# Kernel optimization log

Hardware: AMD Instinct MI355X
Metric: run time of the kernel (lower is better)

Reference implementation:

```python
import jax, jax.numpy as jnp
import numpy as np
import math

B, HW, E = 128, 3136, 96
NH, WS = 3, 7
EH = E // NH
NEG_INF = float('-inf')


def setup_inputs() -> dict:
    key = jax.random.key(0)
    ks = jax.random.split(key, 5)
    x = jax.random.normal(ks[0], (B, HW, E), dtype=jnp.float32)
    w1 = jax.random.normal(ks[1], (3 * E, E), dtype=jnp.float32) * 0.02
    b1 = jnp.zeros((3 * E,), dtype=jnp.float32)
    w2 = jax.random.normal(ks[2], (E, E), dtype=jnp.float32) * 0.02
    b2 = jnp.zeros((E,), dtype=jnp.float32)
    return {"x": x, "w1": w1, "b1": b1, "w2": w2, "b2": b2}


def _masks():
    m = WS * (WS // 2)  # 21
    row = jnp.zeros((WS * WS, WS * WS), dtype=jnp.float32)
    row = row.at[-m:, :-m].set(NEG_INF)
    row = row.at[:-m, -m:].set(NEG_INF)
    # rearrange '(r w1) (c w2) -> (w1 r) (w2 c)'
    col = row.reshape(WS, WS, WS, WS).transpose(1, 0, 3, 2).reshape(WS * WS, WS * WS)
    return row, col


def reference(x, w1, b1, w2, b2):
    b = x.shape[0]
    hh = ww = int(round(math.sqrt(x.shape[1])))
    nh, nw = hh // WS, ww // WS
    qkv = x @ w1.T + b1                      # [b, hw, 3E]
    qkv = qkv.reshape(b, hh, ww, E, 3)       # (c K) split, K=3
    # cyclic shift: (-WS)//2 == -4 (faithful to torch source)
    s = (-WS) // 2
    qkv = jnp.roll(qkv, (s, s), axis=(1, 2))
    # window partition: b (h m1) (w m2) (H E) K -> b H h w (m1 m2) E K
    t = qkv.reshape(b, nh, WS, nw, WS, NH, EH, 3)
    t = t.transpose(0, 5, 1, 3, 2, 4, 6, 7).reshape(b, NH, nh, nw, WS * WS, EH, 3)
    q, k, v = t[..., 0], t[..., 1], t[..., 2]
    att = jnp.einsum('bHxyqe,bHxyke->bHxyqk', q, k) / math.sqrt(EH)
    row_mask, col_mask = _masks()
    att = att.at[:, :, -1, :].add(row_mask)
    att = att.at[:, :, :, -1].add(col_mask)
    p = jax.nn.softmax(att, axis=-1)
    o = jnp.einsum('bHxyqk,bHxyke->bHxyqe', p, v)
    # reverse window partition: b H h w (m1 m2) E -> b (h m1) (w m2) (H E)
    o = o.reshape(b, NH, nh, nw, WS, WS, EH)
    o = o.transpose(0, 2, 4, 3, 5, 1, 6).reshape(b, hh, ww, E)
    o = jnp.roll(o, (WS // 2, WS // 2), axis=(1, 2))  # +3 (faithful)
    o = o.reshape(b, hh * ww, E)
    return o @ w2.T + b2
```

## Files before the change

kernel.cpp:

```cpp
#include <hip/hip_runtime.h>

typedef __attribute__((ext_vector_type(8))) __bf16 bf16x8;
typedef __attribute__((ext_vector_type(4))) float f32x4;
typedef __attribute__((ext_vector_type(4))) unsigned int u32x4;

__device__ __forceinline__ unsigned short f2bf(float f){
    unsigned int x = __builtin_bit_cast(unsigned int, f);
    x += 0x7FFFu + ((x >> 16) & 1u);
    return (unsigned short)(x >> 16);
}
__device__ __forceinline__ unsigned int pk2(float a, float b){
    return (unsigned int)f2bf(a) | ((unsigned int)f2bf(b) << 16);
}
__device__ __forceinline__ unsigned int cvtpk(float a, float b){
    unsigned int r;
    asm("v_cvt_pk_bf16_f32 %0, %1, %2" : "=v"(r) : "v"(a), "v"(b));
    return r;
}
__device__ __forceinline__ unsigned short cvt1(float a){
    return (unsigned short)(cvtpk(a, a) & 0xFFFFu);
}
__device__ __forceinline__ bf16x8 ldfrag(const unsigned short* p){
    u32x4 v = *reinterpret_cast<const u32x4*>(p);
    return __builtin_bit_cast(bf16x8, v);
}
__device__ __forceinline__ bf16x8 ldf32(const float* p){
    f32x4 a = *reinterpret_cast<const f32x4*>(p);
    f32x4 b = *reinterpret_cast<const f32x4*>(p + 4);
    u32x4 r;
    r[0] = cvtpk(a[0], a[1]); r[1] = cvtpk(a[2], a[3]);
    r[2] = cvtpk(b[0], b[1]); r[3] = cvtpk(b[2], b[3]);
    return __builtin_bit_cast(bf16x8, r);
}
__device__ __forceinline__ f32x4 mfma_bf16(bf16x8 a, bf16x8 b, f32x4 c){
    return __builtin_amdgcn_mfma_f32_16x16x32_bf16(a, b, c, 0, 0, 0);
}

#define W1F_SH 27648
#define W2F_SH 9216

__global__ __launch_bounds__(256) void k_prep(const float* __restrict__ w1,
                                              const float* __restrict__ b1,
                                              const float* __restrict__ w2,
                                              unsigned short* __restrict__ w1f,
                                              unsigned short* __restrict__ w2f,
                                              float* __restrict__ b1p)
{
    const float SCALE = 0.17677669529663687f;
    int i = blockIdx.x * 256 + threadIdx.x;
    if (i < 3456){
        int f = i >> 6, lane = i & 63;
        int n = f / 3, ks = f - n * 3;
        int l15 = lane & 15, qd = lane >> 4;
        int rp = n * 16 + l15;
        int c = rp / 96, rem = rp - c * 96;
        float s = (c == 0) ? SCALE : 1.0f;
        const float* src = w1 + (size_t)(3 * rem + c) * 96 + ks * 32 + qd * 8;
        f32x4 v0 = *reinterpret_cast<const f32x4*>(src);
        f32x4 v1 = *reinterpret_cast<const f32x4*>(src + 4);
        u32x4 p;
        p[0] = pk2(v0[0] * s, v0[1] * s); p[1] = pk2(v0[2] * s, v0[3] * s);
        p[2] = pk2(v1[0] * s, v1[1] * s); p[3] = pk2(v1[2] * s, v1[3] * s);
        *reinterpret_cast<u32x4*>(w1f + (size_t)f * 512 + lane * 8) = p;
    } else if (i < 4608){
        int j = i - 3456;
        int f = j >> 6, lane = j & 63;
        int n = f / 3, ks = f - n * 3;
        int l15 = lane & 15, qd = lane >> 4;
        const float* src = w2 + (size_t)(n * 16 + l15) * 96 + ks * 32 + qd * 8;
        f32x4 v0 = *reinterpret_cast<const f32x4*>(src);
        f32x4 v1 = *reinterpret_cast<const f32x4*>(src + 4);
        u32x4 p;
        p[0] = pk2(v0[0], v0[1]); p[1] = pk2(v0[2], v0[3]);
        p[2] = pk2(v1[0], v1[1]); p[3] = pk2(v1[2], v1[3]);
        *reinterpret_cast<u32x4*>(w2f + (size_t)f * 512 + lane * 8) = p;
    } else if (i < 4896){
        int rp = i - 4608;
        int c = rp / 96, rem = rp - c * 96;
        b1p[rp] = b1[3 * rem + c] * ((c == 0) ? SCALE : 1.0f);
    }
}

__global__ __launch_bounds__(256, 6) void k_fused(const float* __restrict__ x,
                                                  const unsigned short* __restrict__ w1f,
                                                  const float* __restrict__ b1p,
                                                  const unsigned short* __restrict__ w2f,
                                                  const float* __restrict__ b2,
                                                  float* __restrict__ out)
{
    __shared__ __align__(16) unsigned short smem[13056];
    unsigned short* Kr = smem;
    unsigned short* Vt = smem + 6144;

    const int tid = threadIdx.x;
    const int win = blockIdx.x;
    const int b = win >> 6, wy = (win >> 3) & 7, wx = win & 7;
    const int wave = tid >> 6, lane = tid & 63;
    const int l15 = lane & 15, qd = lane >> 4;
    const int s0 = (qd & 1) * 32 + l15;
    const int s1 = s0 + 16;

    bf16x8 bQf[3];
    {
        int pos = wave * 16 + l15;
        int iy = pos / 7, ix = pos - iy * 7;
        int h = wy * 7 + iy + 4; if (h >= 56) h -= 56;
        int w = wx * 7 + ix + 4; if (w >= 56) w -= 56;
        const float* xr = x + ((size_t)b * 3136 + h * 56 + w) * 96;
        bf16x8 aX0 = ldf32(xr + qd * 8);
        bf16x8 aX1 = ldf32(xr + 32 + qd * 8);
        bf16x8 aX2 = ldf32(xr + 64 + qd * 8);

        unsigned int Qw[12];
#pragma unroll
        for (int qt = 0; qt < 6; ++qt){
            const unsigned short* wf = w1f + (size_t)(qt * 3) * 512 + lane * 8;
            f32x4 a = {0.f, 0.f, 0.f, 0.f};
            a = mfma_bf16(ldfrag(wf),        aX0, a);
            a = mfma_bf16(ldfrag(wf + 512),  aX1, a);
            a = mfma_bf16(ldfrag(wf + 1024), aX2, a);
            f32x4 bq = *reinterpret_cast<const f32x4*>(b1p + qt * 16 + qd * 4);
            Qw[qt * 2]     = cvtpk(a[0] + bq[0], a[1] + bq[1]);
            Qw[qt * 2 + 1] = cvtpk(a[2] + bq[2], a[3] + bq[3]);
        }
#pragma unroll
        for (int H = 0; H < 3; ++H){
            u32x4 qw; unsigned int lo, hi;
            lo = (unsigned)__shfl((int)Qw[(2*H)*2],     s0, 64);
            hi = (unsigned)__shfl((int)Qw[(2*H+1)*2],   s0, 64); qw[0] = (qd & 2) ? hi : lo;
            lo = (unsigned)__shfl((int)Qw[(2*H)*2+1],   s0, 64);
            hi = (unsigned)__shfl((int)Qw[(2*H+1)*2+1], s0, 64); qw[1] = (qd & 2) ? hi : lo;
            lo = (unsigned)__shfl((int)Qw[(2*H)*2],     s1, 64);
            hi = (unsigned)__shfl((int)Qw[(2*H+1)*2],   s1, 64); qw[2] = (qd & 2) ? hi : lo;
            lo = (unsigned)__shfl((int)Qw[(2*H)*2+1],   s1, 64);
            hi = (unsigned)__shfl((int)Qw[(2*H+1)*2+1], s1, 64); qw[3] = (qd & 2) ? hi : lo;
            bQf[H] = __builtin_bit_cast(bf16x8, qw);
        }

#pragma unroll
        for (int n = 0; n < 6; ++n){
            const unsigned short* wf = w1f + (size_t)((6 + n) * 3) * 512 + lane * 8;
            f32x4 a = {0.f, 0.f, 0.f, 0.f};
            a = mfma_bf16(aX0, ldfrag(wf),        a);
            a = mfma_bf16(aX1, ldfrag(wf + 512),  a);
            a = mfma_bf16(aX2, ldfrag(wf + 1024), a);
            float bb = b1p[(6 + n) * 16 + l15];
            int H = n >> 1;
            int eh = ((n & 1) << 4) + l15;
            int ch = eh >> 3;
#pragma unroll
            for (int r = 0; r < 4; ++r){
                int p = wave * 16 + qd * 4 + r;
                int chs = ch ^ ((p >> 1) & 3);
                Kr[H * 2048 + p * 32 + chs * 8 + (eh & 7)] = cvt1(a[r] + bb);
            }
        }
#pragma unroll
        for (int n = 0; n < 6; ++n){
            const unsigned short* wf = w1f + (size_t)((12 + n) * 3) * 512 + lane * 8;
            f32x4 a = {0.f, 0.f, 0.f, 0.f};
            a = mfma_bf16(aX0, ldfrag(wf),        a);
            a = mfma_bf16(aX1, ldfrag(wf + 512),  a);
            a = mfma_bf16(aX2, ldfrag(wf + 1024), a);
            float bb = b1p[(12 + n) * 16 + l15];
            int H = n >> 1;
            int eh = ((n & 1) << 4) + l15;
            int p0 = wave * 16 + qd * 4;
#pragma unroll
            for (int rp = 0; rp < 2; ++rp)
                *reinterpret_cast<unsigned int*>(&Vt[(H * 32 + eh) * 72 + p0 + 2 * rp])
                    = cvtpk(a[2 * rp] + bb, a[2 * rp + 1] + bb);
        }
    }
    __syncthreads();

    const bool rowm = (wy == 7), colm = (wx == 7);
    const float NEGINF = -__builtin_inff();
    const unsigned int m49 = (qd == 0) ? 0xE000u : 0xF000u;
    const unsigned int m28 = (qd == 3) ? 0xFFF0u : 0xFF00u;
    const unsigned int m7  = (qd & 2) ? ((qd & 1) ? 0x7C03u : 0x03E8u)
                                      : ((qd & 1) ? 0xE817u : 0x17C0u);
    const int qrow = wave * 16 + l15;
    const bool rhi = (qrow >= 28);
    const bool rc7 = ((qrow % 7) >= 4);
    const int chq = qd ^ ((l15 >> 1) & 3);

    unsigned int Ow[12];
#pragma unroll
    for (int H = 0; H < 3; ++H){
        f32x4 S[4];
#pragma unroll
        for (int tn = 0; tn < 4; ++tn){
            bf16x8 aK = ldfrag(Kr + H * 2048 + (tn * 16 + l15) * 32 + chq * 8);
            f32x4 z = {0.f, 0.f, 0.f, 0.f};
            S[tn] = mfma_bf16(aK, bQf[H], z);
        }
        float mx = NEGINF;
#pragma unroll
        for (int tn = 0; tn < 4; ++tn)
#pragma unroll
            for (int r = 0; r < 4; ++r){
                int bit = tn * 4 + r;
                float v = S[tn][r];
                bool blocked = (((m49 >> bit) & 1u) != 0u)
                    || (rowm && (rhi != (((m28 >> bit) & 1u) != 0u)))
                    || (colm && (rc7 != (((m7 >> bit) & 1u) != 0u)));
                v = blocked ? NEGINF : v;
                S[tn][r] = v;
                mx = fmaxf(mx, v);
            }
        mx = fmaxf(mx, __shfl_xor(mx, 16, 64));
        mx = fmaxf(mx, __shfl_xor(mx, 32, 64));
        float sum = 0.f;
#pragma unroll
        for (int tn = 0; tn < 4; ++tn)
#pragma unroll
            for (int r = 0; r < 4; ++r){
                float e = exp2f((S[tn][r] - mx) * 1.4426950408889634f);
                S[tn][r] = e;
                sum += e;
            }
        sum += __shfl_xor(sum, 16, 64);
        sum += __shfl_xor(sum, 32, 64);
        float inv = 1.f / sum;

        unsigned int pkv[8];
#pragma unroll
        for (int tn = 0; tn < 4; ++tn){
            pkv[tn * 2]     = cvtpk(S[tn][0], S[tn][1]);
            pkv[tn * 2 + 1] = cvtpk(S[tn][2], S[tn][3]);
        }
        bf16x8 pF[2];
#pragma unroll
        for (int kt = 0; kt < 2; ++kt){
            u32x4 aw;
#pragma unroll
            for (int w4 = 0; w4 < 4; ++w4){
                int srcl = (w4 < 2) ? s0 : s1;
                unsigned int lo = (unsigned)__shfl((int)pkv[(2 * kt) * 2 + (w4 & 1)], srcl, 64);
                unsigned int hi = (unsigned)__shfl((int)pkv[(2 * kt + 1) * 2 + (w4 & 1)], srcl, 64);
                aw[w4] = (qd & 2) ? hi : lo;
            }
            pF[kt] = __builtin_bit_cast(bf16x8, aw);
        }
#pragma unroll
        for (int et = 0; et < 2; ++et){
            f32x4 o = {0.f, 0.f, 0.f, 0.f};
#pragma unroll
            for (int kt = 0; kt < 2; ++kt){
                bf16x8 aV = ldfrag(Vt + (H * 32 + et * 16 + l15) * 72 + kt * 32 + qd * 8);
                o = mfma_bf16(aV, pF[kt], o);
            }
            Ow[(H * 2 + et) * 2]     = cvtpk(o[0] * inv, o[1] * inv);
            Ow[(H * 2 + et) * 2 + 1] = cvtpk(o[2] * inv, o[3] * inv);
        }
    }

    bf16x8 aO[3];
#pragma unroll
    for (int c = 0; c < 3; ++c){
        u32x4 qw; unsigned int lo, hi;
        lo = (unsigned)__shfl((int)Ow[(2*c)*2],     s0, 64);
        hi = (unsigned)__shfl((int)Ow[(2*c+1)*2],   s0, 64); qw[0] = (qd & 2) ? hi : lo;
        lo = (unsigned)__shfl((int)Ow[(2*c)*2+1],   s0, 64);
        hi = (unsigned)__shfl((int)Ow[(2*c+1)*2+1], s0, 64); qw[1] = (qd & 2) ? hi : lo;
        lo = (unsigned)__shfl((int)Ow[(2*c)*2],     s1, 64);
        hi = (unsigned)__shfl((int)Ow[(2*c+1)*2],   s1, 64); qw[2] = (qd & 2) ? hi : lo;
        lo = (unsigned)__shfl((int)Ow[(2*c)*2+1],   s1, 64);
        hi = (unsigned)__shfl((int)Ow[(2*c+1)*2+1], s1, 64); qw[3] = (qd & 2) ? hi : lo;
        aO[c] = __builtin_bit_cast(bf16x8, qw);
    }

    f32x4 acc2[6];
#pragma unroll
    for (int n = 0; n < 6; ++n){
        const unsigned short* wf = w2f + (size_t)(n * 3) * 512 + lane * 8;
        f32x4 a = {0.f, 0.f, 0.f, 0.f};
        a = mfma_bf16(aO[0], ldfrag(wf),        a);
        a = mfma_bf16(aO[1], ldfrag(wf + 512),  a);
        a = mfma_bf16(aO[2], ldfrag(wf + 1024), a);
        acc2[n] = a;
    }
    float bb2[6];
#pragma unroll
    for (int n = 0; n < 6; ++n) bb2[n] = b2[n * 16 + l15];

#pragma unroll
    for (int r = 0; r < 4; ++r){
        int row = wave * 16 + qd * 4 + r;
        int iy = row / 7, ix = row - iy * 7;
        int h = wy * 7 + iy + 3; if (h >= 56) h -= 56;
        int w = wx * 7 + ix + 3; if (w >= 56) w -= 56;
        float* dst = out + ((size_t)b * 3136 + h * 56 + w) * 96 + l15;
        if (row < 49){
#pragma unroll
            for (int n = 0; n < 6; ++n)
                dst[n * 16] = acc2[n][r] + bb2[n];
        }
    }
}

extern "C" void kernel_launch(void* const* d_in, const int* in_sizes, int n_in,
                              void* d_out, int out_size, void* d_ws, size_t ws_size,
                              hipStream_t stream)
{
    const float* x  = (const float*)d_in[0];
    const float* w1 = (const float*)d_in[1];
    const float* b1 = (const float*)d_in[2];
    const float* w2 = (const float*)d_in[3];
    const float* b2 = (const float*)d_in[4];
    float* out = (float*)d_out;

    unsigned short* w1f = (unsigned short*)d_ws;
    unsigned short* w2f = w1f + W1F_SH;
    float* b1p = (float*)(w2f + W2F_SH);

    hipLaunchKernelGGL(k_prep,  dim3(20),   dim3(256), 0, stream, w1, b1, w2, w1f, w2f, b1p);
    hipLaunchKernelGGL(k_fused, dim3(8192), dim3(256), 0, stream, x, w1f, b1p, w2f, b2, out);
}
```

Before: 364.6 us.

## Process two windows per block with double-buffered LDS and software pipelining

Each block now handles two adjacent windows, using two LDS buffers. The x load and QKV projection for the second window are interleaved with attention and the output projection of the first, so global-load latency and MFMA work can overlap within one block. It also precomputes the additive mask once per thread, restructures the max and sum reductions as trees, and adds s_setprio around the MFMA groups. The cost is more LDS and registers per block, with launch bounds lowered from 6 to 3 blocks per CU and half as many blocks, which reduces occupancy-based latency hiding.

```diff
diff --git a/kernel.cpp b/kernel.cpp
--- a/kernel.cpp
+++ b/kernel.cpp
@@ -23,14 +23,6 @@
 __device__ __forceinline__ bf16x8 ldfrag(const unsigned short* p){
     u32x4 v = *reinterpret_cast<const u32x4*>(p);
     return __builtin_bit_cast(bf16x8, v);
-}
-__device__ __forceinline__ bf16x8 ldf32(const float* p){
-    f32x4 a = *reinterpret_cast<const f32x4*>(p);
-    f32x4 b = *reinterpret_cast<const f32x4*>(p + 4);
-    u32x4 r;
-    r[0] = cvtpk(a[0], a[1]); r[1] = cvtpk(a[2], a[3]);
-    r[2] = cvtpk(b[0], b[1]); r[3] = cvtpk(b[2], b[3]);
-    return __builtin_bit_cast(bf16x8, r);
 }
 __device__ __forceinline__ f32x4 mfma_bf16(bf16x8 a, bf16x8 b, f32x4 c){
     return __builtin_amdgcn_mfma_f32_16x16x32_bf16(a, b, c, 0, 0, 0);
@@ -81,99 +73,104 @@
     }
 }
 
-__global__ __launch_bounds__(256, 6) void k_fused(const float* __restrict__ x,
-                                                  const unsigned short* __restrict__ w1f,
-                                                  const float* __restrict__ b1p,
-                                                  const unsigned short* __restrict__ w2f,
-                                                  const float* __restrict__ b2,
-                                                  float* __restrict__ out)
-{
-    __shared__ __align__(16) unsigned short smem[13056];
-    unsigned short* Kr = smem;
-    unsigned short* Vt = smem + 6144;
-
-    const int tid = threadIdx.x;
-    const int win = blockIdx.x;
-    const int b = win >> 6, wy = (win >> 3) & 7, wx = win & 7;
-    const int wave = tid >> 6, lane = tid & 63;
-    const int l15 = lane & 15, qd = lane >> 4;
-    const int s0 = (qd & 1) * 32 + l15;
-    const int s1 = s0 + 16;
-
-    bf16x8 bQf[3];
-    {
-        int pos = wave * 16 + l15;
-        int iy = pos / 7, ix = pos - iy * 7;
-        int h = wy * 7 + iy + 4; if (h >= 56) h -= 56;
-        int w = wx * 7 + ix + 4; if (w >= 56) w -= 56;
-        const float* xr = x + ((size_t)b * 3136 + h * 56 + w) * 96;
-        bf16x8 aX0 = ldf32(xr + qd * 8);
-        bf16x8 aX1 = ldf32(xr + 32 + qd * 8);
-        bf16x8 aX2 = ldf32(xr + 64 + qd * 8);
-
-        unsigned int Qw[12];
-#pragma unroll
-        for (int qt = 0; qt < 6; ++qt){
-            const unsigned short* wf = w1f + (size_t)(qt * 3) * 512 + lane * 8;
-            f32x4 a = {0.f, 0.f, 0.f, 0.f};
-            a = mfma_bf16(ldfrag(wf),        aX0, a);
-            a = mfma_bf16(ldfrag(wf + 512),  aX1, a);
-            a = mfma_bf16(ldfrag(wf + 1024), aX2, a);
-            f32x4 bq = *reinterpret_cast<const f32x4*>(b1p + qt * 16 + qd * 4);
-            Qw[qt * 2]     = cvtpk(a[0] + bq[0], a[1] + bq[1]);
-            Qw[qt * 2 + 1] = cvtpk(a[2] + bq[2], a[3] + bq[3]);
-        }
-#pragma unroll
-        for (int H = 0; H < 3; ++H){
-            u32x4 qw; unsigned int lo, hi;
-            lo = (unsigned)__shfl((int)Qw[(2*H)*2],     s0, 64);
-            hi = (unsigned)__shfl((int)Qw[(2*H+1)*2],   s0, 64); qw[0] = (qd & 2) ? hi : lo;
-            lo = (unsigned)__shfl((int)Qw[(2*H)*2+1],   s0, 64);
-            hi = (unsigned)__shfl((int)Qw[(2*H+1)*2+1], s0, 64); qw[1] = (qd & 2) ? hi : lo;
-            lo = (unsigned)__shfl((int)Qw[(2*H)*2],     s1, 64);
-            hi = (unsigned)__shfl((int)Qw[(2*H+1)*2],   s1, 64); qw[2] = (qd & 2) ? hi : lo;
-            lo = (unsigned)__shfl((int)Qw[(2*H)*2+1],   s1, 64);
-            hi = (unsigned)__shfl((int)Qw[(2*H+1)*2+1], s1, 64); qw[3] = (qd & 2) ? hi : lo;
-            bQf[H] = __builtin_bit_cast(bf16x8, qw);
-        }
-
-#pragma unroll
-        for (int n = 0; n < 6; ++n){
-            const unsigned short* wf = w1f + (size_t)((6 + n) * 3) * 512 + lane * 8;
-            f32x4 a = {0.f, 0.f, 0.f, 0.f};
-            a = mfma_bf16(aX0, ldfrag(wf),        a);
-            a = mfma_bf16(aX1, ldfrag(wf + 512),  a);
-            a = mfma_bf16(aX2, ldfrag(wf + 1024), a);
-            float bb = b1p[(6 + n) * 16 + l15];
-            int H = n >> 1;
-            int eh = ((n & 1) << 4) + l15;
-            int ch = eh >> 3;
-#pragma unroll
-            for (int r = 0; r < 4; ++r){
-                int p = wave * 16 + qd * 4 + r;
-                int chs = ch ^ ((p >> 1) & 3);
-                Kr[H * 2048 + p * 32 + chs * 8 + (eh & 7)] = cvt1(a[r] + bb);
-            }
-        }
-#pragma unroll
-        for (int n = 0; n < 6; ++n){
-            const unsigned short* wf = w1f + (size_t)((12 + n) * 3) * 512 + lane * 8;
-            f32x4 a = {0.f, 0.f, 0.f, 0.f};
-            a = mfma_bf16(aX0, ldfrag(wf),        a);
-            a = mfma_bf16(aX1, ldfrag(wf + 512),  a);
-            a = mfma_bf16(aX2, ldfrag(wf + 1024), a);
-            float bb = b1p[(12 + n) * 16 + l15];
-            int H = n >> 1;
-            int eh = ((n & 1) << 4) + l15;
-            int p0 = wave * 16 + qd * 4;
-#pragma unroll
-            for (int rp = 0; rp < 2; ++rp)
-                *reinterpret_cast<unsigned int*>(&Vt[(H * 32 + eh) * 72 + p0 + 2 * rp])
-                    = cvtpk(a[2 * rp] + bb, a[2 * rp + 1] + bb);
-        }
-    }
-    __syncthreads();
-
+
+__device__ __forceinline__ void load_x_raw(const float* __restrict__ x, int b, int wy, int wx,
+                                           int wave, int l15, int qd, f32x4* xv)
+{
+    int pos = wave * 16 + l15;
+    int iy = pos / 7, ix = pos - iy * 7;
+    int h = wy * 7 + iy + 4; if (h >= 56) h -= 56;
+    int w = wx * 7 + ix + 4; if (w >= 56) w -= 56;
+    const float* xr = x + ((size_t)b * 3136 + h * 56 + w) * 96 + qd * 8;
+    xv[0] = *reinterpret_cast<const f32x4*>(xr);
+    xv[1] = *reinterpret_cast<const f32x4*>(xr + 4);
+    xv[2] = *reinterpret_cast<const f32x4*>(xr + 32);
+    xv[3] = *reinterpret_cast<const f32x4*>(xr + 36);
+    xv[4] = *reinterpret_cast<const f32x4*>(xr + 64);
+    xv[5] = *reinterpret_cast<const f32x4*>(xr + 68);
+}
+
+__device__ __forceinline__ void compute_A(const f32x4* xv,
+    const unsigned short* __restrict__ w1f, const float* __restrict__ b1p,
+    unsigned short* Kr, unsigned short* Vt,
+    int wave, int lane, int l15, int qd, int s0, int s1, bf16x8* bQf)
+{
+    u32x4 t;
+    t[0] = cvtpk(xv[0][0], xv[0][1]); t[1] = cvtpk(xv[0][2], xv[0][3]);
+    t[2] = cvtpk(xv[1][0], xv[1][1]); t[3] = cvtpk(xv[1][2], xv[1][3]);
+    bf16x8 aX0 = __builtin_bit_cast(bf16x8, t);
+    t[0] = cvtpk(xv[2][0], xv[2][1]); t[1] = cvtpk(xv[2][2], xv[2][3]);
+    t[2] = cvtpk(xv[3][0], xv[3][1]); t[3] = cvtpk(xv[3][2], xv[3][3]);
+    bf16x8 aX1 = __builtin_bit_cast(bf16x8, t);
+    t[0] = cvtpk(xv[4][0], xv[4][1]); t[1] = cvtpk(xv[4][2], xv[4][3]);
+    t[2] = cvtpk(xv[5][0], xv[5][1]); t[3] = cvtpk(xv[5][2], xv[5][3]);
+    bf16x8 aX2 = __builtin_bit_cast(bf16x8, t);
+
+    unsigned int Qw[12];
+#pragma unroll
+    for (int qt = 0; qt < 6; ++qt){
+        const unsigned short* wf = w1f + (size_t)(qt * 3) * 512 + lane * 8;
+        f32x4 a = {0.f, 0.f, 0.f, 0.f};
+        a = mfma_bf16(ldfrag(wf),        aX0, a);
+        a = mfma_bf16(ldfrag(wf + 512),  aX1, a);
+        a = mfma_bf16(ldfrag(wf + 1024), aX2, a);
+        f32x4 bq = *reinterpret_cast<const f32x4*>(b1p + qt * 16 + qd * 4);
+        Qw[qt * 2]     = cvtpk(a[0] + bq[0], a[1] + bq[1]);
+        Qw[qt * 2 + 1] = cvtpk(a[2] + bq[2], a[3] + bq[3]);
+    }
+#pragma unroll
+    for (int H = 0; H < 3; ++H){
+        u32x4 qw; unsigned int lo, hi;
+        lo = (unsigned)__shfl((int)Qw[(2*H)*2],     s0, 64);
+        hi = (unsigned)__shfl((int)Qw[(2*H+1)*2],   s0, 64); qw[0] = (qd & 2) ? hi : lo;
+        lo = (unsigned)__shfl((int)Qw[(2*H)*2+1],   s0, 64);
+        hi = (unsigned)__shfl((int)Qw[(2*H+1)*2+1], s0, 64); qw[1] = (qd & 2) ? hi : lo;
+        lo = (unsigned)__shfl((int)Qw[(2*H)*2],     s1, 64);
+        hi = (unsigned)__shfl((int)Qw[(2*H+1)*2],   s1, 64); qw[2] = (qd & 2) ? hi : lo;
+        lo = (unsigned)__shfl((int)Qw[(2*H)*2+1],   s1, 64);
+        hi = (unsigned)__shfl((int)Qw[(2*H+1)*2+1], s1, 64); qw[3] = (qd & 2) ? hi : lo;
+        bQf[H] = __builtin_bit_cast(bf16x8, qw);
+    }
+#pragma unroll
+    for (int n = 0; n < 6; ++n){
+        const unsigned short* wf = w1f + (size_t)((6 + n) * 3) * 512 + lane * 8;
+        f32x4 a = {0.f, 0.f, 0.f, 0.f};
+        a = mfma_bf16(aX0, ldfrag(wf),        a);
+        a = mfma_bf16(aX1, ldfrag(wf + 512),  a);
+        a = mfma_bf16(aX2, ldfrag(wf + 1024), a);
+        float bb = b1p[(6 + n) * 16 + l15];
+        int H = n >> 1;
+        int eh = ((n & 1) << 4) + l15;
+        int ch = eh >> 3;
+#pragma unroll
+        for (int r = 0; r < 4; ++r){
+            int p = wave * 16 + qd * 4 + r;
+            int chs = ch ^ ((p >> 1) & 3);
+            Kr[H * 2048 + p * 32 + chs * 8 + (eh & 7)] = cvt1(a[r] + bb);
+        }
+    }
+#pragma unroll
+    for (int n = 0; n < 6; ++n){
+        const unsigned short* wf = w1f + (size_t)((12 + n) * 3) * 512 + lane * 8;
+        f32x4 a = {0.f, 0.f, 0.f, 0.f};
+        a = mfma_bf16(aX0, ldfrag(wf),        a);
+        a = mfma_bf16(aX1, ldfrag(wf + 512),  a);
+        a = mfma_bf16(aX2, ldfrag(wf + 1024), a);
+        float bb = b1p[(12 + n) * 16 + l15];
+        int H = n >> 1;
+        int eh = ((n & 1) << 4) + l15;
+        int p0 = wave * 16 + qd * 4;
+#pragma unroll
+        for (int rp = 0; rp < 2; ++rp)
+            *reinterpret_cast<unsigned int*>(&Vt[(H * 32 + eh) * 72 + p0 + 2 * rp])
+                = cvtpk(a[2 * rp] + bb, a[2 * rp + 1] + bb);
+    }
+}
+
+__device__ __forceinline__ void phase_B(const unsigned short* Kr, const unsigned short* Vt,
+    const bf16x8* bQf, int wy, int wx, int wave, int l15, int qd, int s0, int s1, int chq,
+    bf16x8* aO)
+{
     const bool rowm = (wy == 7), colm = (wx == 7);
     const float NEGINF = -__builtin_inff();
     const unsigned int m49 = (qd == 0) ? 0xE000u : 0xF000u;
@@ -183,43 +180,51 @@
     const int qrow = wave * 16 + l15;
     const bool rhi = (qrow >= 28);
     const bool rc7 = ((qrow % 7) >= 4);
-    const int chq = qd ^ ((l15 >> 1) & 3);
+    float madd[16];
+#pragma unroll
+    for (int bit = 0; bit < 16; ++bit){
+        bool blocked = (((m49 >> bit) & 1u) != 0u)
+            || (rowm && (rhi != (((m28 >> bit) & 1u) != 0u)))
+            || (colm && (rc7 != (((m7 >> bit) & 1u) != 0u)));
+        madd[bit] = blocked ? NEGINF : 0.f;
+    }
 
     unsigned int Ow[12];
 #pragma unroll
     for (int H = 0; H < 3; ++H){
         f32x4 S[4];
+        __builtin_amdgcn_s_setprio(1);
 #pragma unroll
         for (int tn = 0; tn < 4; ++tn){
             bf16x8 aK = ldfrag(Kr + H * 2048 + (tn * 16 + l15) * 32 + chq * 8);
             f32x4 z = {0.f, 0.f, 0.f, 0.f};
             S[tn] = mfma_bf16(aK, bQf[H], z);
         }
-        float mx = NEGINF;
+        __builtin_amdgcn_s_setprio(0);
+        float v[16];
 #pragma unroll
         for (int tn = 0; tn < 4; ++tn)
 #pragma unroll
-            for (int r = 0; r < 4; ++r){
-                int bit = tn * 4 + r;
-                float v = S[tn][r];
-                bool blocked = (((m49 >> bit) & 1u) != 0u)
-                    || (rowm && (rhi != (((m28 >> bit) & 1u) != 0u)))
-                    || (colm && (rc7 != (((m7 >> bit) & 1u) != 0u)));
-                v = blocked ? NEGINF : v;
-                S[tn][r] = v;
-                mx = fmaxf(mx, v);
-            }
+            for (int r = 0; r < 4; ++r)
+                v[tn * 4 + r] = S[tn][r] + madd[tn * 4 + r];
+        float a0 = fmaxf(fmaxf(v[0], v[1]),  v[2]);
+        float a1 = fmaxf(fmaxf(v[3], v[4]),  v[5]);
+        float a2 = fmaxf(fmaxf(v[6], v[7]),  v[8]);
+        float a3 = fmaxf(fmaxf(v[9], v[10]), v[11]);
+        float a4 = fmaxf(fmaxf(v[12], v[13]), v[14]);
+        float mx = fmaxf(fmaxf(fmaxf(a0, a1), a2), fmaxf(fmaxf(a3, a4), v[15]));
         mx = fmaxf(mx, __shfl_xor(mx, 16, 64));
         mx = fmaxf(mx, __shfl_xor(mx, 32, 64));
-        float sum = 0.f;
-#pragma unroll
-        for (int tn = 0; tn < 4; ++tn)
-#pragma unroll
-            for (int r = 0; r < 4; ++r){
-                float e = exp2f((S[tn][r] - mx) * 1.4426950408889634f);
-                S[tn][r] = e;
-                sum += e;
-            }
+        float e[16];
+#pragma unroll
+        for (int i = 0; i < 16; ++i) e[i] = exp2f((v[i] - mx) * 1.4426950408889634f);
+        float t8[8];
+#pragma unroll
+        for (int i = 0; i < 8; ++i) t8[i] = e[2 * i] + e[2 * i + 1];
+        float t4[4];
+#pragma unroll
+        for (int i = 0; i < 4; ++i) t4[i] = t8[2 * i] + t8[2 * i + 1];
+        float sum = (t4[0] + t4[1]) + (t4[2] + t4[3]);
         sum += __shfl_xor(sum, 16, 64);
         sum += __shfl_xor(sum, 32, 64);
         float inv = 1.f / sum;
@@ -227,8 +232,8 @@
         unsigned int pkv[8];
 #pragma unroll
         for (int tn = 0; tn < 4; ++tn){
-            pkv[tn * 2]     = cvtpk(S[tn][0], S[tn][1]);
-            pkv[tn * 2 + 1] = cvtpk(S[tn][2], S[tn][3]);
+            pkv[tn * 2]     = cvtpk(e[tn * 4 + 0], e[tn * 4 + 1]);
+            pkv[tn * 2 + 1] = cvtpk(e[tn * 4 + 2], e[tn * 4 + 3]);
         }
         bf16x8 pF[2];
 #pragma unroll
@@ -246,17 +251,17 @@
 #pragma unroll
         for (int et = 0; et < 2; ++et){
             f32x4 o = {0.f, 0.f, 0.f, 0.f};
+            __builtin_amdgcn_s_setprio(1);
 #pragma unroll
             for (int kt = 0; kt < 2; ++kt){
                 bf16x8 aV = ldfrag(Vt + (H * 32 + et * 16 + l15) * 72 + kt * 32 + qd * 8);
                 o = mfma_bf16(aV, pF[kt], o);
             }
+            __builtin_amdgcn_s_setprio(0);
             Ow[(H * 2 + et) * 2]     = cvtpk(o[0] * inv, o[1] * inv);
             Ow[(H * 2 + et) * 2 + 1] = cvtpk(o[2] * inv, o[3] * inv);
         }
     }
-
-    bf16x8 aO[3];
 #pragma unroll
     for (int c = 0; c < 3; ++c){
         u32x4 qw; unsigned int lo, hi;
@@ -270,7 +275,12 @@
         hi = (unsigned)__shfl((int)Ow[(2*c+1)*2+1], s1, 64); qw[3] = (qd & 2) ? hi : lo;
         aO[c] = __builtin_bit_cast(bf16x8, qw);
     }
-
+}
+
+__device__ __forceinline__ void phase_C(const bf16x8* aO,
+    const unsigned short* __restrict__ w2f, const float* __restrict__ b2,
+    float* __restrict__ out, int b, int wy, int wx, int wave, int lane, int l15, int qd)
+{
     f32x4 acc2[6];
 #pragma unroll
     for (int n = 0; n < 6; ++n){
@@ -284,7 +294,6 @@
     float bb2[6];
 #pragma unroll
     for (int n = 0; n < 6; ++n) bb2[n] = b2[n * 16 + l15];
-
 #pragma unroll
     for (int r = 0; r < 4; ++r){
         int row = wave * 16 + qd * 4 + r;
@@ -300,6 +309,44 @@
     }
 }
 
+__global__ __launch_bounds__(256, 3) void k_fused(const float* __restrict__ x,
+                                                  const unsigned short* __restrict__ w1f,
+                                                  const float* __restrict__ b1p,
+                                                  const unsigned short* __restrict__ w2f,
+                                                  const float* __restrict__ b2,
+                                                  float* __restrict__ out)
+{
+    __shared__ __align__(16) unsigned short smem[2][13056];
+
+    const int tid = threadIdx.x;
+    const int w0 = blockIdx.x * 2;
+    const int b = w0 >> 6, wy = (w0 >> 3) & 7, wx0 = w0 & 7, wx1 = wx0 + 1;
+    const int wave = tid >> 6, lane = tid & 63;
+    const int l15 = lane & 15, qd = lane >> 4;
+    const int s0 = (qd & 1) * 32 + l15;
+    const int s1 = s0 + 16;
+    const int chq = qd ^ ((l15 >> 1) & 3);
+
+    f32x4 xv0[6];
+    load_x_raw(x, b, wy, wx0, wave, l15, qd, xv0);
+    bf16x8 bQf0[3];
+    compute_A(xv0, w1f, b1p, smem[0], smem[0] + 6144, wave, lane, l15, qd, s0, s1, bQf0);
+    __syncthreads();
+
+    f32x4 xv1[6];
+    load_x_raw(x, b, wy, wx1, wave, l15, qd, xv1);
+    bf16x8 aO0[3];
+    phase_B(smem[0], smem[0] + 6144, bQf0, wy, wx0, wave, l15, qd, s0, s1, chq, aO0);
+    bf16x8 bQf1[3];
+    compute_A(xv1, w1f, b1p, smem[1], smem[1] + 6144, wave, lane, l15, qd, s0, s1, bQf1);
+    phase_C(aO0, w2f, b2, out, b, wy, wx0, wave, lane, l15, qd);
+    __syncthreads();
+
+    bf16x8 aO1[3];
+    phase_B(smem[1], smem[1] + 6144, bQf1, wy, wx1, wave, l15, qd, s0, s1, chq, aO1);
+    phase_C(aO1, w2f, b2, out, b, wy, wx1, wave, lane, l15, qd);
+}
+
 extern "C" void kernel_launch(void* const* d_in, const int* in_sizes, int n_in,
                               void* d_out, int out_size, void* d_ws, size_t ws_size,
                               hipStream_t stream)
@@ -316,5 +363,5 @@
     float* b1p = (float*)(w2f + W2F_SH);
 
     hipLaunchKernelGGL(k_prep,  dim3(20),   dim3(256), 0, stream, w1, b1, w2, w1f, w2f, b1p);
-    hipLaunchKernelGGL(k_fused, dim3(8192), dim3(256), 0, stream, x, w1f, b1p, w2f, b2, out);
-}
+    hipLaunchKernelGGL(k_fused, dim3(4096), dim3(256), 0, stream, x, w1f, b1p, w2f, b2, out);
+}
```

Result: no change. 364.9 us (+0.1%).
